# Optimization experiments

Measured on AMD Instinct MI355X. Metric: run time of the kernel, lower is better.

The kernel has to match this reference:

```python
import jax, jax.numpy as jnp
import numpy as np

D_ATT = 256
D_GROUP = 32
N_GROUP = D_ATT // D_GROUP


def setup_inputs() -> dict:
    key = jax.random.key(0)
    ks = jax.random.split(key, 6)
    B, L = 4, 512
    import math
    s = 1.0 / math.sqrt(D_ATT)
    return {
        "x": jax.random.normal(ks[0], (B, L, D_ATT), dtype=jnp.float32),
        "Wq": jax.random.normal(ks[1], (D_ATT, D_ATT), dtype=jnp.float32) * s * 0.06,
        "Wk": jax.random.normal(ks[2], (D_ATT, D_ATT), dtype=jnp.float32) * s * 0.06,
        "Wv": jax.random.normal(ks[3], (D_ATT, D_ATT), dtype=jnp.float32) * s * 0.06,
        "w_mlp": jax.random.normal(ks[4], (D_GROUP,), dtype=jnp.float32) * 0.1,
        "b_mlp": jax.random.normal(ks[5], (1,), dtype=jnp.float32) * 0.1,
    }


def reference(x, Wq, Wk, Wv, w_mlp, b_mlp):
    B, L, d_att = x.shape
    G, Dg = N_GROUP, D_GROUP
    # nn.Linear(bias=False): y = x @ W.T
    Q = x @ Wq.T  # (B, L, d_att)
    K = x @ Wk.T
    V = x @ Wv.T
    Qg = Q.reshape(B, L, 1, G, Dg)
    Kg = K.reshape(B, 1, L, G, Dg)
    # group_MLP: ReLU -> Linear(Dg, 1) -> ReLU, applied to Q-K diff
    # diff: (B, Lq, Lk, G, Dg) -- the huge intermediate a fused kernel would avoid
    diff = Qg - Kg
    attn = jnp.einsum('bqkgd,d->bqkg', jax.nn.relu(diff), w_mlp) + b_mlp[0]
    attn = jax.nn.relu(attn)
    # positional_adding_bias=0, positional_multiplying_bias=1 (defaults), no mask
    attn = jax.nn.softmax(attn, axis=2)  # softmax over key positions
    # NOTE: original views V as (B, L, d_group, n_group) -- asymmetric grouping, kept faithful
    Vg = V.reshape(B, L, Dg, G)
    out = jnp.einsum('bqkg,bkdg->bqdg', attn, Vg)  # (B, Lq, Dg, G)
    return out.reshape(B, L, d_att)
```

## Files before the change

kernel.cpp:

```cpp
#include <hip/hip_runtime.h>

typedef float f32x2 __attribute__((ext_vector_type(2)));
typedef float f32x4 __attribute__((ext_vector_type(4)));
typedef short bf16x8 __attribute__((ext_vector_type(8)));
typedef _Float16 h16x2 __attribute__((ext_vector_type(2)));
typedef _Float16 h16x8 __attribute__((ext_vector_type(8)));

#define LL 512
#define M_ROWS 2048
#define KC 768

#if __has_builtin(__builtin_amdgcn_exp2f)
#define EXP2F __builtin_amdgcn_exp2f
#else
#define EXP2F exp2f
#endif
#define LOG2E 1.44269504088896340736f

__device__ __forceinline__ float quad_swap1(float x) {
    return __int_as_float(__builtin_amdgcn_mov_dpp(__float_as_int(x), 0xB1, 0xF, 0xF, true));
}
__device__ __forceinline__ float quad_swap2(float x) {
    return __int_as_float(__builtin_amdgcn_mov_dpp(__float_as_int(x), 0x4E, 0xF, 0xF, true));
}

__device__ __forceinline__ float fdot2f(h16x2 a, h16x2 b, float c) {
#if __has_builtin(__builtin_amdgcn_fdot2)
    return __builtin_amdgcn_fdot2(a, b, c, false);
#else
    return fmaf((float)a.x, (float)b.x, fmaf((float)a.y, (float)b.y, c));
#endif
}

__device__ __forceinline__ unsigned short bf16_rtne(float x) {
    unsigned u = __float_as_uint(x);
    return (unsigned short)((u + 0x7fffu + ((u >> 16) & 1u)) >> 16);
}
__device__ __forceinline__ float bf16_to_f(unsigned short h) {
    return __uint_as_float((unsigned)h << 16);
}

__global__ __launch_bounds__(64) void split_bf16(
    const float* __restrict__ X, const float* __restrict__ Wq,
    const float* __restrict__ Wk, const float* __restrict__ Wv,
    unsigned short* __restrict__ Xc, unsigned short* __restrict__ Wc)
{
    const int row = blockIdx.x;
    const int t = threadIdx.x;
    const float* src;
    unsigned short* hi1; unsigned short* hi2; unsigned short* lo1;
    if (row < M_ROWS) {
        src = X + (size_t)row * 256;
        hi1 = Xc + (size_t)row * KC;
        hi2 = hi1 + 256;
        lo1 = hi1 + 512;
    } else {
        const int n = row - M_ROWS;
        const int mat = n >> 8, c = n & 255;
        const int srow = (mat == 2) ? (((c & 31) << 3) | (c >> 5)) : c;
        src = (mat == 0 ? Wq : (mat == 1 ? Wk : Wv)) + (size_t)srow * 256;
        hi1 = Wc + (size_t)n * KC;
        lo1 = hi1 + 256;
        hi2 = hi1 + 512;
    }
    const f32x4 v = *(const f32x4*)(src + t * 4);
    ushort4 h, l;
    h.x = bf16_rtne(v.x); h.y = bf16_rtne(v.y); h.z = bf16_rtne(v.z); h.w = bf16_rtne(v.w);
    l.x = bf16_rtne(v.x - bf16_to_f(h.x));
    l.y = bf16_rtne(v.y - bf16_to_f(h.y));
    l.z = bf16_rtne(v.z - bf16_to_f(h.z));
    l.w = bf16_rtne(v.w - bf16_to_f(h.w));
    *(ushort4*)(hi1 + t * 4) = h;
    *(ushort4*)(hi2 + t * 4) = h;
    *(ushort4*)(lo1 + t * 4) = l;
}

__global__ __launch_bounds__(64) void qkv_mfma(
    const unsigned short* __restrict__ Xc, const unsigned short* __restrict__ Wc,
    _Float16* __restrict__ Qh, _Float16* __restrict__ Kh, float* __restrict__ Vt)
{
    const int bid = blockIdx.x;
    const int m0 = (bid & 31) * 64;
    const int n0 = (bid >> 5) * 64;
    const int l = threadIdx.x;
    const int lr = l & 15;
    const int lk = (l >> 4) * 8;

    size_t aoff[4], boff[4];
#pragma unroll
    for (int i = 0; i < 4; ++i) {
        aoff[i] = (size_t)(m0 + i * 16 + lr) * KC + lk;
        boff[i] = (size_t)(n0 + i * 16 + lr) * KC + lk;
    }

    f32x4 acc[4][4];
#pragma unroll
    for (int i = 0; i < 4; ++i)
#pragma unroll
        for (int j = 0; j < 4; ++j) acc[i][j] = (f32x4){0.f, 0.f, 0.f, 0.f};

    bf16x8 A0[4], B0[4], A1[4], B1[4];
#pragma unroll
    for (int i = 0; i < 4; ++i) {
        A0[i] = *(const bf16x8*)(Xc + aoff[i]);
        B0[i] = *(const bf16x8*)(Wc + boff[i]);
    }

#pragma unroll 1
    for (int it = 0; it < 24; it += 2) {
        const int ks1 = (it + 1) * 32;
#pragma unroll
        for (int i = 0; i < 4; ++i) {
            A1[i] = *(const bf16x8*)(Xc + aoff[i] + ks1);
            B1[i] = *(const bf16x8*)(Wc + boff[i] + ks1);
        }
#pragma unroll
        for (int ai = 0; ai < 4; ++ai)
#pragma unroll
            for (int bi = 0; bi < 4; ++bi)
                acc[ai][bi] = __builtin_amdgcn_mfma_f32_16x16x32_bf16(
                    A0[ai], B0[bi], acc[ai][bi], 0, 0, 0);
        if (it + 2 < 24) {
            const int ks2 = (it + 2) * 32;
#pragma unroll
            for (int i = 0; i < 4; ++i) {
                A0[i] = *(const bf16x8*)(Xc + aoff[i] + ks2);
                B0[i] = *(const bf16x8*)(Wc + boff[i] + ks2);
            }
        }
#pragma unroll
        for (int ai = 0; ai < 4; ++ai)
#pragma unroll
            for (int bi = 0; bi < 4; ++bi)
                acc[ai][bi] = __builtin_amdgcn_mfma_f32_16x16x32_bf16(
                    A1[ai], B1[bi], acc[ai][bi], 0, 0, 0);
    }

    const int mat = n0 >> 8;
    if (mat == 2) {
#pragma unroll
        for (int ai = 0; ai < 4; ++ai)
#pragma unroll
            for (int bi = 0; bi < 4; ++bi) {
                const int col = (n0 & 255) + bi * 16 + lr;
#pragma unroll
                for (int r = 0; r < 4; ++r) {
                    const int row = m0 + ai * 16 + (l >> 4) * 4 + r;
                    Vt[(size_t)row * 256 + col] = acc[ai][bi][r];
                }
            }
    } else {
        _Float16* Hb = (mat == 0) ? Qh : Kh;
#pragma unroll
        for (int ai = 0; ai < 4; ++ai)
#pragma unroll
            for (int bi = 0; bi < 4; ++bi) {
                const int col = (n0 & 255) + bi * 16 + lr;
#pragma unroll
                for (int r = 0; r < 4; ++r) {
                    const int row = m0 + ai * 16 + (l >> 4) * 4 + r;
                    Hb[(size_t)row * 256 + col] = (_Float16)acc[ai][bi][r];
                }
            }
    }
}

__global__ __launch_bounds__(512, 4) void attn_fused(
    const _Float16* __restrict__ Qh, const _Float16* __restrict__ Kh,
    const float* __restrict__ Vt,
    const float* __restrict__ w_mlp, const float* __restrict__ b_mlp,
    float* __restrict__ out)
{
    const int bid = blockIdx.x;
    const int b = bid & 3;
    const int q0 = (bid >> 2) * 4;

    const int t = threadIdx.x;
    const int dh = t & 3;
    const int p = t >> 5;
    const int lane32 = t & 31;
    const int g = lane32 >> 2;

    __shared__ float accbuf[16][32][37];

    const int doff = g * 32 + dh * 8;
    const float bias4 = b_mlp[0] * (LOG2E * 0.25f);

    h16x2 w2[4];
    {
        f32x4 wa = *(const f32x4*)(w_mlp + dh * 8);
        f32x4 wb = *(const f32x4*)(w_mlp + dh * 8 + 4);
        wa *= LOG2E; wb *= LOG2E;
        w2[0] = (h16x2){(_Float16)wa.x, (_Float16)wa.y};
        w2[1] = (h16x2){(_Float16)wa.z, (_Float16)wa.w};
        w2[2] = (h16x2){(_Float16)wb.x, (_Float16)wb.y};
        w2[3] = (h16x2){(_Float16)wb.z, (_Float16)wb.w};
    }

    h16x2 qr2[4][4];
#pragma unroll
    for (int q = 0; q < 4; ++q) {
        const h16x8 qv = *(const h16x8*)(Qh + ((size_t)(b * LL) + q0 + q) * 256 + doff);
        qr2[q][0] = __builtin_shufflevector(qv, qv, 0, 1);
        qr2[q][1] = __builtin_shufflevector(qv, qv, 2, 3);
        qr2[q][2] = __builtin_shufflevector(qv, qv, 4, 5);
        qr2[q][3] = __builtin_shufflevector(qv, qv, 6, 7);
    }

    f32x2 acc2[4][4];
#pragma unroll
    for (int q = 0; q < 4; ++q)
#pragma unroll
        for (int j = 0; j < 4; ++j) acc2[q][j] = (f32x2){0.f, 0.f};
    float l[4] = {0.f, 0.f, 0.f, 0.f};

    const _Float16* kptr = Kh + ((size_t)(b * LL) + p) * 256 + doff;
    const float* vptr = Vt + ((size_t)(b * LL) + p) * 256 + doff;

    const h16x2 zh = {(_Float16)0.f, (_Float16)0.f};

    auto compute = [&](h16x8 kv, f32x4 va, f32x4 vb) {
        h16x2 k2[4] = {__builtin_shufflevector(kv, kv, 0, 1),
                       __builtin_shufflevector(kv, kv, 2, 3),
                       __builtin_shufflevector(kv, kv, 4, 5),
                       __builtin_shufflevector(kv, kv, 6, 7)};
        f32x2 v2[4] = {__builtin_shufflevector(va, va, 0, 1),
                       __builtin_shufflevector(va, va, 2, 3),
                       __builtin_shufflevector(vb, vb, 0, 1),
                       __builtin_shufflevector(vb, vb, 2, 3)};
#pragma unroll
        for (int q = 0; q < 4; ++q) {
            float s = bias4;
#pragma unroll
            for (int j = 0; j < 4; ++j) {
                h16x2 d2 = qr2[q][j] - k2[j];
                h16x2 r2 = __builtin_elementwise_max(d2, zh);
                s = fdot2f(w2[j], r2, s);
            }
            s += quad_swap1(s);
            s += quad_swap2(s);
            s = fmaxf(s, 0.f);
            const float e = EXP2F(s);
            l[q] += e;
            const f32x2 e2 = {e, e};
#pragma unroll
            for (int j = 0; j < 4; ++j) acc2[q][j] += e2 * v2[j];
        }
    };

    h16x8 kc = *(const h16x8*)kptr;
    f32x4 va = *(const f32x4*)vptr, vb = *(const f32x4*)(vptr + 4);
#pragma unroll 1
    for (int i = 0; i < 31; ++i) {
        kptr += 16 * 256; vptr += 16 * 256;
        h16x8 kn = *(const h16x8*)kptr;
        f32x4 va2 = *(const f32x4*)vptr, vb2 = *(const f32x4*)(vptr + 4);
        compute(kc, va, vb);
        kc = kn; va = va2; vb = vb2;
    }
    compute(kc, va, vb);

    {
        float* rowp = &accbuf[p][lane32][0];
#pragma unroll
        for (int qq = 0; qq < 4; ++qq)
#pragma unroll
            for (int j = 0; j < 4; ++j)
                *(f32x2*)(rowp + qq * 8 + j * 2) = acc2[qq][j];
        if (dh == 0) {
#pragma unroll
            for (int qq = 0; qq < 4; ++qq) accbuf[p][lane32][32 + qq] = l[qq];
        }
    }
    __syncthreads();

    const int c_o = t & 255;
    const int g_o = c_o & 7, d_o = c_o >> 3;
    const int rowb = g_o * 4 + (d_o >> 3);
    const int colb = d_o & 7;
    const int qsel = t >> 8;
#pragma unroll
    for (int h = 0; h < 2; ++h) {
        const int qh = qsel + 2 * h;
        float s = 0.f, ls = 0.f;
#pragma unroll
        for (int pp = 0; pp < 16; ++pp) {
            s  += accbuf[pp][rowb][qh * 8 + colb];
            ls += accbuf[pp][g_o * 4][32 + qh];
        }
        out[((size_t)(b * LL) + q0 + qh) * 256 + c_o] = s / ls;
    }
}

extern "C" void kernel_launch(void* const* d_in, const int* in_sizes, int n_in,
                              void* d_out, int out_size, void* d_ws, size_t ws_size,
                              hipStream_t stream) {
    (void)in_sizes; (void)n_in; (void)out_size; (void)ws_size;
    const float* x     = (const float*)d_in[0];
    const float* Wq    = (const float*)d_in[1];
    const float* Wk    = (const float*)d_in[2];
    const float* Wv    = (const float*)d_in[3];
    const float* w_mlp = (const float*)d_in[4];
    const float* b_mlp = (const float*)d_in[5];
    float* outp = (float*)d_out;

    _Float16* Qh = (_Float16*)d_ws;
    _Float16* Kh = (_Float16*)((char*)d_ws + (size_t)1048576);
    float*    Vt = (float*)((char*)d_ws + (size_t)2097152);
    unsigned short* Xc = (unsigned short*)((char*)d_ws + (size_t)6291456);
    unsigned short* Wc = (unsigned short*)((char*)d_ws + (size_t)6291456 + 3145728);

    split_bf16<<<dim3(M_ROWS + 768), 64, 0, stream>>>(x, Wq, Wk, Wv, Xc, Wc);
    qkv_mfma<<<dim3(384), 64, 0, stream>>>(Xc, Wc, Qh, Kh, Vt);
    attn_fused<<<dim3(512), 512, 0, stream>>>(Qh, Kh, Vt, w_mlp, b_mlp, outp);
}
```

Before: 118.2 us.

## Replace bf16 split plus MFMA projection with single fp32 tiled SIMT GEMM

Drops the split_bf16 pre-pass and the bf16x3 MFMA GEMM and computes the QKV projection in one fp32 shared-memory tiled GEMM that reads x and the weights directly. This removes a kernel launch and the round trip of the split buffers through memory. The cost is that the GEMM now runs on vector FP32 ALUs instead of matrix cores. It also rewrites the attention PV accumulation as explicit FMA.

New measurement: 110.3 us. 1.07x faster.

```diff
diff --git a/kernel.cpp b/kernel.cpp
--- a/kernel.cpp
+++ b/kernel.cpp
@@ -2,13 +2,12 @@
 
 typedef float f32x2 __attribute__((ext_vector_type(2)));
 typedef float f32x4 __attribute__((ext_vector_type(4)));
-typedef short bf16x8 __attribute__((ext_vector_type(8)));
 typedef _Float16 h16x2 __attribute__((ext_vector_type(2)));
+typedef _Float16 h16x4 __attribute__((ext_vector_type(4)));
 typedef _Float16 h16x8 __attribute__((ext_vector_type(8)));
 
 #define LL 512
 #define M_ROWS 2048
-#define KC 768
 
 #if __has_builtin(__builtin_amdgcn_exp2f)
 #define EXP2F __builtin_amdgcn_exp2f
@@ -32,136 +31,102 @@
 #endif
 }
 
-__device__ __forceinline__ unsigned short bf16_rtne(float x) {
-    unsigned u = __float_as_uint(x);
-    return (unsigned short)((u + 0x7fffu + ((u >> 16) & 1u)) >> 16);
-}
-__device__ __forceinline__ float bf16_to_f(unsigned short h) {
-    return __uint_as_float((unsigned)h << 16);
-}
-
-__global__ __launch_bounds__(64) void split_bf16(
+__global__ __launch_bounds__(128) void qkv_gemm(
     const float* __restrict__ X, const float* __restrict__ Wq,
     const float* __restrict__ Wk, const float* __restrict__ Wv,
-    unsigned short* __restrict__ Xc, unsigned short* __restrict__ Wc)
-{
-    const int row = blockIdx.x;
-    const int t = threadIdx.x;
-    const float* src;
-    unsigned short* hi1; unsigned short* hi2; unsigned short* lo1;
-    if (row < M_ROWS) {
-        src = X + (size_t)row * 256;
-        hi1 = Xc + (size_t)row * KC;
-        hi2 = hi1 + 256;
-        lo1 = hi1 + 512;
-    } else {
-        const int n = row - M_ROWS;
-        const int mat = n >> 8, c = n & 255;
-        const int srow = (mat == 2) ? (((c & 31) << 3) | (c >> 5)) : c;
-        src = (mat == 0 ? Wq : (mat == 1 ? Wk : Wv)) + (size_t)srow * 256;
-        hi1 = Wc + (size_t)n * KC;
-        lo1 = hi1 + 256;
-        hi2 = hi1 + 512;
-    }
-    const f32x4 v = *(const f32x4*)(src + t * 4);
-    ushort4 h, l;
-    h.x = bf16_rtne(v.x); h.y = bf16_rtne(v.y); h.z = bf16_rtne(v.z); h.w = bf16_rtne(v.w);
-    l.x = bf16_rtne(v.x - bf16_to_f(h.x));
-    l.y = bf16_rtne(v.y - bf16_to_f(h.y));
-    l.z = bf16_rtne(v.z - bf16_to_f(h.z));
-    l.w = bf16_rtne(v.w - bf16_to_f(h.w));
-    *(ushort4*)(hi1 + t * 4) = h;
-    *(ushort4*)(hi2 + t * 4) = h;
-    *(ushort4*)(lo1 + t * 4) = l;
-}
-
-__global__ __launch_bounds__(64) void qkv_mfma(
-    const unsigned short* __restrict__ Xc, const unsigned short* __restrict__ Wc,
     _Float16* __restrict__ Qh, _Float16* __restrict__ Kh, float* __restrict__ Vt)
 {
-    const int bid = blockIdx.x;
-    const int m0 = (bid & 31) * 64;
-    const int n0 = (bid >> 5) * 64;
-    const int l = threadIdx.x;
-    const int lr = l & 15;
-    const int lk = (l >> 4) * 8;
-
-    size_t aoff[4], boff[4];
-#pragma unroll
-    for (int i = 0; i < 4; ++i) {
-        aoff[i] = (size_t)(m0 + i * 16 + lr) * KC + lk;
-        boff[i] = (size_t)(n0 + i * 16 + lr) * KC + lk;
-    }
-
-    f32x4 acc[4][4];
-#pragma unroll
-    for (int i = 0; i < 4; ++i)
-#pragma unroll
-        for (int j = 0; j < 4; ++j) acc[i][j] = (f32x4){0.f, 0.f, 0.f, 0.f};
-
-    bf16x8 A0[4], B0[4], A1[4], B1[4];
-#pragma unroll
-    for (int i = 0; i < 4; ++i) {
-        A0[i] = *(const bf16x8*)(Xc + aoff[i]);
-        B0[i] = *(const bf16x8*)(Wc + boff[i]);
-    }
-
-#pragma unroll 1
-    for (int it = 0; it < 24; it += 2) {
-        const int ks1 = (it + 1) * 32;
+    const int bx = blockIdx.x;
+    const int by = blockIdx.y;
+    const int mat = bx >> 2;
+    const int n0 = (bx & 3) * 64;
+    const int m0 = by * 32;
+    const float* W = (mat == 0) ? Wq : (mat == 1 ? Wk : Wv);
+
+    __shared__ float As[2][32][36];
+    __shared__ float Bs[2][32][68];
+
+    const int t = threadIdx.x;
+    const int tx = t & 15;
+    const int ty = t >> 4;
+
+    int am[2], ak4[2];
+#pragma unroll
+    for (int r = 0; r < 2; ++r) { int idx = t + 128 * r; am[r] = idx >> 3; ak4[r] = idx & 7; }
+    int bn[4], bk4[4]; size_t brow[4];
+#pragma unroll
+    for (int r = 0; r < 4; ++r) {
+        int idx = t + 128 * r; bn[r] = idx >> 3; bk4[r] = idx & 7;
+        int rowc = n0 + bn[r];
+        brow[r] = (mat == 2) ? (size_t)(((rowc & 31) << 3) | (rowc >> 5)) : (size_t)rowc;
+    }
+
+    f32x4 arg[2], brg[4];
+    auto load_tile = [&](int kc) {
+#pragma unroll
+        for (int r = 0; r < 2; ++r)
+            arg[r] = *(const f32x4*)(X + (size_t)(m0 + am[r]) * 256 + kc + ak4[r] * 4);
+#pragma unroll
+        for (int r = 0; r < 4; ++r)
+            brg[r] = *(const f32x4*)(W + brow[r] * 256 + kc + bk4[r] * 4);
+    };
+    auto store_tile = [&](int buf) {
+#pragma unroll
+        for (int r = 0; r < 2; ++r)
+#pragma unroll
+            for (int j = 0; j < 4; ++j) As[buf][ak4[r] * 4 + j][am[r]] = arg[r][j];
+#pragma unroll
+        for (int r = 0; r < 4; ++r)
+#pragma unroll
+            for (int j = 0; j < 4; ++j) Bs[buf][bk4[r] * 4 + j][bn[r]] = brg[r][j];
+    };
+
+    load_tile(0);
+    store_tile(0);
+    __syncthreads();
+
+    f32x2 c[4][2];
+#pragma unroll
+    for (int i = 0; i < 4; ++i) { c[i][0] = (f32x2){0.f, 0.f}; c[i][1] = (f32x2){0.f, 0.f}; }
+
+    for (int it = 0; it < 8; ++it) {
+        const int buf = it & 1;
+        if (it < 7) load_tile((it + 1) * 32);
+#pragma unroll
+        for (int kk = 0; kk < 32; ++kk) {
+            const f32x4 a4 = *(const f32x4*)&As[buf][kk][ty * 4];
+            const f32x4 b4 = *(const f32x4*)&Bs[buf][kk][tx * 4];
+            const f32x2 bl = __builtin_shufflevector(b4, b4, 0, 1);
+            const f32x2 bh = __builtin_shufflevector(b4, b4, 2, 3);
+#pragma unroll
+            for (int i = 0; i < 4; ++i) {
+                const f32x2 ai = {a4[i], a4[i]};
+                c[i][0] += ai * bl;
+                c[i][1] += ai * bh;
+            }
+        }
+        if (it < 7) {
+            __syncthreads();
+            store_tile(buf ^ 1);
+            __syncthreads();
+        }
+    }
+
+    const int colb = n0 + tx * 4;
+    if (mat == 2) {
 #pragma unroll
         for (int i = 0; i < 4; ++i) {
-            A1[i] = *(const bf16x8*)(Xc + aoff[i] + ks1);
-            B1[i] = *(const bf16x8*)(Wc + boff[i] + ks1);
-        }
-#pragma unroll
-        for (int ai = 0; ai < 4; ++ai)
-#pragma unroll
-            for (int bi = 0; bi < 4; ++bi)
-                acc[ai][bi] = __builtin_amdgcn_mfma_f32_16x16x32_bf16(
-                    A0[ai], B0[bi], acc[ai][bi], 0, 0, 0);
-        if (it + 2 < 24) {
-            const int ks2 = (it + 2) * 32;
-#pragma unroll
-            for (int i = 0; i < 4; ++i) {
-                A0[i] = *(const bf16x8*)(Xc + aoff[i] + ks2);
-                B0[i] = *(const bf16x8*)(Wc + boff[i] + ks2);
-            }
-        }
-#pragma unroll
-        for (int ai = 0; ai < 4; ++ai)
-#pragma unroll
-            for (int bi = 0; bi < 4; ++bi)
-                acc[ai][bi] = __builtin_amdgcn_mfma_f32_16x16x32_bf16(
-                    A1[ai], B1[bi], acc[ai][bi], 0, 0, 0);
-    }
-
-    const int mat = n0 >> 8;
-    if (mat == 2) {
-#pragma unroll
-        for (int ai = 0; ai < 4; ++ai)
-#pragma unroll
-            for (int bi = 0; bi < 4; ++bi) {
-                const int col = (n0 & 255) + bi * 16 + lr;
-#pragma unroll
-                for (int r = 0; r < 4; ++r) {
-                    const int row = m0 + ai * 16 + (l >> 4) * 4 + r;
-                    Vt[(size_t)row * 256 + col] = acc[ai][bi][r];
-                }
-            }
+            f32x4 v = {c[i][0].x, c[i][0].y, c[i][1].x, c[i][1].y};
+            *(f32x4*)(Vt + (size_t)(m0 + ty * 4 + i) * 256 + colb) = v;
+        }
     } else {
         _Float16* Hb = (mat == 0) ? Qh : Kh;
 #pragma unroll
-        for (int ai = 0; ai < 4; ++ai)
-#pragma unroll
-            for (int bi = 0; bi < 4; ++bi) {
-                const int col = (n0 & 255) + bi * 16 + lr;
-#pragma unroll
-                for (int r = 0; r < 4; ++r) {
-                    const int row = m0 + ai * 16 + (l >> 4) * 4 + r;
-                    Hb[(size_t)row * 256 + col] = (_Float16)acc[ai][bi][r];
-                }
-            }
+        for (int i = 0; i < 4; ++i) {
+            h16x4 hv = {(_Float16)c[i][0].x, (_Float16)c[i][0].y,
+                        (_Float16)c[i][1].x, (_Float16)c[i][1].y};
+            *(h16x4*)(Hb + (size_t)(m0 + ty * 4 + i) * 256 + colb) = hv;
+        }
     }
 }
 
@@ -244,7 +209,8 @@
             l[q] += e;
             const f32x2 e2 = {e, e};
 #pragma unroll
-            for (int j = 0; j < 4; ++j) acc2[q][j] += e2 * v2[j];
+            for (int j = 0; j < 4; ++j)
+                acc2[q][j] = __builtin_elementwise_fma(v2[j], e2, acc2[q][j]);
         }
     };
 
@@ -307,10 +273,7 @@
     _Float16* Qh = (_Float16*)d_ws;
     _Float16* Kh = (_Float16*)((char*)d_ws + (size_t)1048576);
     float*    Vt = (float*)((char*)d_ws + (size_t)2097152);
-    unsigned short* Xc = (unsigned short*)((char*)d_ws + (size_t)6291456);
-    unsigned short* Wc = (unsigned short*)((char*)d_ws + (size_t)6291456 + 3145728);
-
-    split_bf16<<<dim3(M_ROWS + 768), 64, 0, stream>>>(x, Wq, Wk, Wv, Xc, Wc);
-    qkv_mfma<<<dim3(384), 64, 0, stream>>>(Xc, Wc, Qh, Kh, Vt);
+
+    qkv_gemm<<<dim3(12, 64), 128, 0, stream>>>(x, Wq, Wk, Wv, Qh, Kh, Vt);
     attn_fused<<<dim3(512), 512, 0, stream>>>(Qh, Kh, Vt, w_mlp, b_mlp, outp);
 }
```
